# Optimization experiments

Hardware: AMD Instinct MI355X
Metric: run time of the kernel (lower is better)

## Reference

```python
import jax, jax.numpy as jnp
import numpy as np

V, C, S, H, B, T = 10000, 1024, 128, 256, 16, 128
NEG = -1e10


def _mlp(x, w1, b1, w2, b2, wo, bo):
    # ResidualLayer (dropout=0, eval): relu(lin1) -> relu(lin2 + residual), then final Linear
    h = jax.nn.relu(x @ w1 + b1)
    h = jax.nn.relu(h @ w2 + b2 + x)
    return h @ wo + bo


def setup_inputs() -> dict:
    key = jax.random.key(0)
    ks = iter(jax.random.split(key, 32))
    d = {}
    d["text"] = jax.random.randint(next(ks), (B, T), 0, V)
    d["word2state"] = jax.random.randint(next(ks), (V, S), 0, C)

    def rn(shape, scale):
        return jax.random.normal(next(ks), shape, dtype=jnp.float32) * scale

    s = 1.0 / np.sqrt(H)
    d["start_emb"] = rn((C, H), 1.0)
    d["start_w1"], d["start_b1"] = rn((H, H), s), jnp.zeros((H,), jnp.float32)
    d["start_w2"], d["start_b2"] = rn((H, H), s), jnp.zeros((H,), jnp.float32)
    d["start_wo"], d["start_bo"] = rn((H, 1), s), jnp.zeros((1,), jnp.float32)
    d["state_emb"] = rn((C, H), 1.0)
    d["trans_w1"], d["trans_b1"] = rn((H, H), s), jnp.zeros((H,), jnp.float32)
    d["trans_w2"], d["trans_b2"] = rn((H, H), s), jnp.zeros((H,), jnp.float32)
    d["trans_wo"], d["trans_bo"] = rn((H, C), s), jnp.zeros((C,), jnp.float32)
    d["pre_emb"] = rn((C, H), 1.0)
    d["term_w1"], d["term_b1"] = rn((H, H), s), jnp.zeros((H,), jnp.float32)
    d["term_w2"], d["term_b2"] = rn((H, H), s), jnp.zeros((H,), jnp.float32)
    d["term_wo"], d["term_bo"] = rn((H, V), s), jnp.zeros((V,), jnp.float32)
    return d


def _evidence(text, word2state,
              start_emb, start_w1, start_b1, start_w2, start_b2, start_wo, start_bo,
              state_emb, trans_w1, trans_b1, trans_w2, trans_b2, trans_wo, trans_bo,
              pre_emb, term_w1, term_b1, term_w2, term_b2, term_wo, term_bo):
    # start distribution over C states
    start = jax.nn.log_softmax(
        _mlp(start_emb, start_w1, start_b1, start_w2, start_b2, start_wo, start_bo)[:, 0])
    # transition [C, C]
    transition = jax.nn.log_softmax(
        _mlp(state_emb, trans_w1, trans_b1, trans_w2, trans_b2, trans_wo, trans_bo), axis=-1)
    # emission with sparse state->word mask (scatter of word2state)
    em_logits = _mlp(pre_emb, term_w1, term_b1, term_w2, term_b2, term_wo, term_bo)  # [C, V]
    a = jnp.repeat(jnp.arange(V), S)  # word index per (word, slot)
    mask = jnp.zeros((C, V), dtype=bool).at[word2state.reshape(-1), a].set(True)
    emission = jax.nn.log_softmax(jnp.where(mask, em_logits, NEG), axis=-1)  # [C, V]

    clamped = word2state[text]  # [B, T, S] states allowed per token
    init = start[clamped[:, 0]]  # [B, S]
    # transition restricted to clamped states: [B, T-1, S_prev, S_next]
    lp = transition[clamped[:, :-1, :, None], clamped[:, 1:, None, :]]
    obs = emission[clamped, text[:, :, None]]  # [B, T, S]
    lp = lp + obs[:, 1:, None, :]                     # emission of next token
    lp = lp.at[:, 0].add(init[:, :, None] + obs[:, 0, :, None])
    lp = jnp.swapaxes(lp, -1, -2)  # [B, T-1, S_next, S_prev]

    # forward algorithm (log-space scan)
    alpha = jax.nn.logsumexp(lp[:, 0], axis=-1)  # [B, S]
    pots = jnp.swapaxes(lp[:, 1:], 0, 1)  # [T-2, B, S, S]

    def step(a_prev, pot):
        return jax.nn.logsumexp(pot + a_prev[:, None, :], axis=-1), None

    alpha_T, _ = jax.lax.scan(step, alpha, pots)
    return jax.nn.logsumexp(alpha_T, axis=-1).sum()


def reference(text, word2state,
              start_emb, start_w1, start_b1, start_w2, start_b2, start_wo, start_bo,
              state_emb, trans_w1, trans_b1, trans_w2, trans_b2, trans_wo, trans_bo,
              pre_emb, term_w1, term_b1, term_w2, term_b2, term_wo, term_bo):
    return _evidence(text, word2state,
                     start_emb, start_w1, start_b1, start_w2, start_b2, start_wo, start_bo,
                     state_emb, trans_w1, trans_b1, trans_w2, trans_b2, trans_wo, trans_bo,
                     pre_emb, term_w1, term_b1, term_w2, term_b2, term_wo, term_bo)
```

## Files before the change

kernel.cpp:

```cpp
#include <hip/hip_runtime.h>
#include <hip/hip_bf16.h>

#define V 10000
#define VP 10112
#define C 1024
#define S 128
#define H 256
#define B 16
#define T 128
#define NR 64
#define CHUNK 158
#define NRP 158
#define LDK 40
#define PITCH 136

typedef unsigned short u16;
typedef unsigned int u32;
typedef __bf16 bf16x8 __attribute__((ext_vector_type(8)));
typedef float f32x4 __attribute__((ext_vector_type(4)));

static __device__ __forceinline__ float bf2f(u16 x){ return __uint_as_float(((u32)x)<<16); }
static __device__ __forceinline__ u16 f2bf(float f){ u32 u=__float_as_uint(f); return (u16)((u + 0x7FFFu + ((u>>16)&1u))>>16); }

struct Cvt3 { const float* s0; const float* s1; const float* s2; u16* d0; u16* d1; u16* d2; };
__global__ __launch_bounds__(256) void k_cvt3(Cvt3 a){
  const float* s = (blockIdx.y==0)? a.s0 : (blockIdx.y==1)? a.s1 : a.s2;
  u16* d = (blockIdx.y==0)? a.d0 : (blockIdx.y==1)? a.d1 : a.d2;
  int i = (blockIdx.x*256 + threadIdx.x)*8;
  float4 x0 = *(const float4*)(s+i);
  float4 x1 = *(const float4*)(s+i+4);
  u16 h[8] = {f2bf(x0.x),f2bf(x0.y),f2bf(x0.z),f2bf(x0.w),f2bf(x1.x),f2bf(x1.y),f2bf(x1.z),f2bf(x1.w)};
  *(uint4*)(d+i) = *(uint4*)h;
}

__global__ __launch_bounds__(256) void k_transpose(const float* __restrict__ src, u16* __restrict__ dst, int N){
  __shared__ float tile[32][33];
  int v0 = blockIdx.x*32, k0 = blockIdx.y*32;
  int tx = threadIdx.x, ty = threadIdx.y;
  for (int i=0;i<32;i+=8){
    int k = k0+ty+i, v = v0+tx;
    tile[ty+i][tx] = (v < N) ? src[(size_t)k*N + v] : 0.f;
  }
  __syncthreads();
  for (int i=0;i<32;i+=8){
    int v = v0+ty+i, k = k0+tx;
    dst[(size_t)v*H + k] = f2bf(tile[tx][ty+i]);
  }
}

struct T6 { const float* s[6]; u16* d[6]; };
__global__ __launch_bounds__(256) void k_transpose6(T6 a){
  const float* src = a.s[blockIdx.z];
  u16* dst = a.d[blockIdx.z];
  __shared__ float tile[32][33];
  int v0 = blockIdx.x*32, k0 = blockIdx.y*32;
  int tx = threadIdx.x, ty = threadIdx.y;
  for (int i=0;i<32;i+=8){
    int k = k0+ty+i, v = v0+tx;
    tile[ty+i][tx] = src[(size_t)k*H + v];
  }
  __syncthreads();
  for (int i=0;i<32;i+=8){
    int v = v0+ty+i, k = k0+tx;
    dst[(size_t)v*H + k] = f2bf(tile[tx][ty+i]);
  }
}

struct M3 { const u16* A[3]; const u16* W[3]; const float* bias[3]; const u16* R[3]; u16* O[3]; };
template<int RESID>
__global__ __launch_bounds__(256) void k_mlpg(M3 a){
  const int z = blockIdx.z;
  const u16* A  = a.A[z];
  const u16* BT = a.W[z];
  const float* bias = a.bias[z];
  const u16* Rm = a.R[z];
  u16* O = a.O[z];
  __shared__ u16 As[128*LDK];
  __shared__ u16 Bs[128*LDK];
  const int tid = threadIdx.x;
  const int lane = tid & 63, wave = tid >> 6;
  const int wm = wave >> 1, wn = wave & 1;
  const int m0 = blockIdx.y * 128, n0 = blockIdx.x * 128;
  const int lr = lane & 15, lg = lane >> 4;
  f32x4 acc[4][4] = {};
  const int sr = tid >> 1, sh = (tid & 1) * 16;
  for (int ks = 0; ks < H; ks += 32){
    const u16* ga = A  + (size_t)(m0 + sr)*H + ks + sh;
    const u16* gb = BT + (size_t)(n0 + sr)*H + ks + sh;
    uint4 a0 = *(const uint4*)ga;
    uint4 a1 = *(const uint4*)(ga + 8);
    uint4 b0 = *(const uint4*)gb;
    uint4 b1 = *(const uint4*)(gb + 8);
    __syncthreads();
    *(uint4*)&As[sr*LDK + sh]     = a0;
    *(uint4*)&As[sr*LDK + sh + 8] = a1;
    *(uint4*)&Bs[sr*LDK + sh]     = b0;
    *(uint4*)&Bs[sr*LDK + sh + 8] = b1;
    __syncthreads();
    bf16x8 af[4], bfr[4];
    #pragma unroll
    for (int m=0;m<4;m++) af[m]  = *(const bf16x8*)&As[(wm*64 + m*16 + lr)*LDK + lg*8];
    #pragma unroll
    for (int n=0;n<4;n++) bfr[n] = *(const bf16x8*)&Bs[(wn*64 + n*16 + lr)*LDK + lg*8];
    #pragma unroll
    for (int m=0;m<4;m++)
      #pragma unroll
      for (int n=0;n<4;n++)
        acc[m][n] = __builtin_amdgcn_mfma_f32_16x16x32_bf16(af[m], bfr[n], acc[m][n], 0,0,0);
  }
  #pragma unroll
  for (int m=0;m<4;m++){
    int r_g = m0 + wm*64 + m*16 + lg*4;
    #pragma unroll
    for (int n=0;n<4;n++){
      int n_g = n0 + wn*64 + n*16 + lr;
      float bv = bias[n_g];
      #pragma unroll
      for (int reg=0; reg<4; reg++){
        int r = r_g + reg;
        float val = acc[m][n][reg] + bv;
        if (RESID) val += bf2f(Rm[(size_t)r*H + n_g]);
        val = fmaxf(val, 0.f);
        O[(size_t)r*H + n_g] = f2bf(val);
      }
    }
  }
}

__global__ __launch_bounds__(1024) void k_start(
    const u16* __restrict__ h2, const float* __restrict__ wo, const float* __restrict__ bo,
    float* __restrict__ start_lp){
  const int c = threadIdx.x;
  const int lane = c & 63, wid = c >> 6;
  __shared__ float red[16];
  __shared__ float Ms, Zs;
  float acc = bo[0];
  const u16* row = h2 + (size_t)c*H;
  for (int k=0;k<H;k+=8){
    uint4 hv = *(const uint4*)(row+k);
    float4 w0 = *(const float4*)(wo+k);
    float4 w1 = *(const float4*)(wo+k+4);
    acc = fmaf(bf2f((u16)(hv.x&0xFFFFu)), w0.x, acc);
    acc = fmaf(bf2f((u16)(hv.x>>16)),     w0.y, acc);
    acc = fmaf(bf2f((u16)(hv.y&0xFFFFu)), w0.z, acc);
    acc = fmaf(bf2f((u16)(hv.y>>16)),     w0.w, acc);
    acc = fmaf(bf2f((u16)(hv.z&0xFFFFu)), w1.x, acc);
    acc = fmaf(bf2f((u16)(hv.z>>16)),     w1.y, acc);
    acc = fmaf(bf2f((u16)(hv.w&0xFFFFu)), w1.z, acc);
    acc = fmaf(bf2f((u16)(hv.w>>16)),     w1.w, acc);
  }
  float m = acc;
  for (int o=1;o<64;o<<=1) m = fmaxf(m, __shfl_xor(m,o));
  if (lane==0) red[wid]=m;
  __syncthreads();
  if (c==0){ float t=red[0]; for(int i=1;i<16;i++) t=fmaxf(t,red[i]); Ms=t; }
  __syncthreads();
  float M = Ms;
  float e = expf(acc - M);
  float sum = e;
  for (int o=1;o<64;o<<=1) sum += __shfl_xor(sum,o);
  __syncthreads();
  if (lane==0) red[wid]=sum;
  __syncthreads();
  if (c==0){ float t=0.f; for(int i=0;i<16;i++) t+=red[i]; Zs=t; }
  __syncthreads();
  start_lp[c] = acc - (M + logf(Zs));
}

template<int BIAS_ROW, int BF16OUT, int COLMAX>
__global__ __launch_bounds__(256) void k_gemm(
    const u16* __restrict__ A, const u16* __restrict__ BT,
    const float* __restrict__ bias, int biasBound,
    void* __restrict__ outp, int ldout, float* __restrict__ cmax){
  __shared__ u16 As[128*LDK];
  __shared__ u16 Bs[128*LDK];
  const int tid = threadIdx.x;
  const int lane = tid & 63, wave = tid >> 6;
  const int wm = wave >> 1, wn = wave & 1;
  const int m0 = blockIdx.y * 128, n0 = blockIdx.x * 128;
  const int lr = lane & 15, lg = lane >> 4;
  f32x4 acc[4][4] = {};
  const int sr = tid >> 1, sh = (tid & 1) * 16;
  for (int ks = 0; ks < H; ks += 32){
    const u16* ga = A  + (size_t)(m0 + sr)*H + ks + sh;
    const u16* gb = BT + (size_t)(n0 + sr)*H + ks + sh;
    uint4 a0 = *(const uint4*)ga;
    uint4 a1 = *(const uint4*)(ga + 8);
    uint4 b0 = *(const uint4*)gb;
    uint4 b1 = *(const uint4*)(gb + 8);
    __syncthreads();
    *(uint4*)&As[sr*LDK + sh]     = a0;
    *(uint4*)&As[sr*LDK + sh + 8] = a1;
    *(uint4*)&Bs[sr*LDK + sh]     = b0;
    *(uint4*)&Bs[sr*LDK + sh + 8] = b1;
    __syncthreads();
    bf16x8 af[4], bfr[4];
    #pragma unroll
    for (int m=0;m<4;m++) af[m]  = *(const bf16x8*)&As[(wm*64 + m*16 + lr)*LDK + lg*8];
    #pragma unroll
    for (int n=0;n<4;n++) bfr[n] = *(const bf16x8*)&Bs[(wn*64 + n*16 + lr)*LDK + lg*8];
    #pragma unroll
    for (int m=0;m<4;m++)
      #pragma unroll
      for (int n=0;n<4;n++)
        acc[m][n] = __builtin_amdgcn_mfma_f32_16x16x32_bf16(af[m], bfr[n], acc[m][n], 0,0,0);
  }
  float cmx[4] = {-1e30f,-1e30f,-1e30f,-1e30f};
  #pragma unroll
  for (int m=0;m<4;m++){
    int r_g = m0 + wm*64 + m*16 + lg*4;
    #pragma unroll
    for (int n=0;n<4;n++){
      int n_g = n0 + wn*64 + n*16 + lr;
      float bcol = BIAS_ROW ? 0.f : bias[n_g];
      #pragma unroll
      for (int reg=0; reg<4; reg++){
        int r = r_g + reg;
        float bv = BIAS_ROW ? ((r < biasBound) ? bias[r] : 0.f) : bcol;
        float val = acc[m][n][reg] + bv;
        if (COLMAX) cmx[n] = fmaxf(cmx[n], val);
        if (BF16OUT) ((u16*)outp)[(size_t)r*ldout + n_g] = f2bf(val);
        else         ((float*)outp)[(size_t)r*ldout + n_g] = val;
      }
    }
  }
  if (COLMAX){
    #pragma unroll
    for (int n=0;n<4;n++){
      float m_ = cmx[n];
      m_ = fmaxf(m_, __shfl_xor(m_,16));
      m_ = fmaxf(m_, __shfl_xor(m_,32));
      if (lg==0) cmax[((size_t)(blockIdx.y*2 + wm))*C + n0 + wn*64 + n*16 + lr] = m_;
    }
  }
}

__global__ __launch_bounds__(256) void k_softmax(const float* __restrict__ TL, u16* __restrict__ P){
  const int c = blockIdx.x;
  const int tid = threadIdx.x, lane = tid & 63, wid = tid >> 6;
  __shared__ float red[4];
  __shared__ float Ms, Zs;
  float4 v = ((const float4*)(TL + (size_t)c*C))[tid];
  float m = fmaxf(fmaxf(v.x,v.y), fmaxf(v.z,v.w));
  for (int o=1;o<64;o<<=1) m = fmaxf(m, __shfl_xor(m,o));
  if (lane==0) red[wid] = m;
  __syncthreads();
  if (tid==0) Ms = fmaxf(fmaxf(red[0],red[1]), fmaxf(red[2],red[3]));
  __syncthreads();
  float M = Ms;
  float e0 = expf(v.x-M), e1 = expf(v.y-M), e2 = expf(v.z-M), e3 = expf(v.w-M);
  float s = (e0+e1)+(e2+e3);
  for (int o=1;o<64;o<<=1) s += __shfl_xor(s,o);
  if (lane==0) red[wid] = s;
  __syncthreads();
  if (tid==0) Zs = red[0]+red[1]+red[2]+red[3];
  __syncthreads();
  float inv = 1.f/Zs;
  u32 lo = (u32)f2bf(e0*inv) | ((u32)f2bf(e1*inv)<<16);
  u32 hi = (u32)f2bf(e2*inv) | ((u32)f2bf(e3*inv)<<16);
  *(uint2*)(P + (size_t)c*C + tid*4) = make_uint2(lo, hi);
}

__global__ void k_shiftc(const float* __restrict__ shiftp, float* __restrict__ shift){
  int c = threadIdx.x + blockIdx.x*blockDim.x;
  if (c < C){
    float m = -1e30f;
    for (int r=0;r<NRP;r++) m = fmaxf(m, shiftp[(size_t)r*C + c]);
    shift[c] = m;
  }
}

__global__ __launch_bounds__(256) void k_scatter(
    const int* __restrict__ w2s, const u16* __restrict__ EM,
    const float* __restrict__ shift, u16* __restrict__ D){
  int idx = blockIdx.x*256 + threadIdx.x;
  int v = idx >> 7;
  const int c = w2s[idx];
  float val = bf2f(EM[(size_t)v*C + c]);
  D[(size_t)v*C + c] = f2bf(expf(val - shift[c]));
}

__global__ __launch_bounds__(256) void k_colsum(const u16* __restrict__ D, float* __restrict__ sumexp){
  const int c = blockIdx.x*256 + threadIdx.x;
  const int v0 = blockIdx.y*CHUNK;
  float s = 0.f;
  const u16* p = D + (size_t)v0*C + c;
  #pragma unroll 2
  for (int i=0;i<CHUNK;i++){ s += bf2f(p[0]); p += C; }
  sumexp[(size_t)blockIdx.y*C + c] = s;
}

__global__ void k_lse(const float* __restrict__ shift, const float* __restrict__ sumexp, float* __restrict__ lse){
  int c = threadIdx.x + blockIdx.x*blockDim.x;
  if (c < C){
    float s = 0.f;
    for (int r=0;r<NR;r++) s += sumexp[(size_t)r*C + c];
    lse[c] = shift[c] + logf(s);
  }
}

__global__ __launch_bounds__(128) void k_obs(
    const int* __restrict__ text, const int* __restrict__ w2s,
    const u16* __restrict__ EM, const float* __restrict__ lse,
    float* __restrict__ obs){
  const int bt = blockIdx.x;
  const int s = threadIdx.x;
  const int v = text[bt];
  const int c = w2s[(size_t)v*S + s];
  obs[(size_t)bt*S + s] = bf2f(EM[(size_t)v*C + c]) - lse[c];
}

__global__ __launch_bounds__(256) void k_pair0(
    const int* __restrict__ text, const int* __restrict__ w2s,
    const float* __restrict__ start_lp, const float* __restrict__ obs,
    const u16* __restrict__ P, u16* __restrict__ out, float* __restrict__ scales){
  const int j = blockIdx.x;
  const int b = blockIdx.y;
  const int t0 = 2*j, t1 = 2*j+1;
  __shared__ __align__(16) u16 tile[128*PITCH];
  __shared__ int cp0[S], cn0[S], cp1[S], cn1[S];
  __shared__ float eo0[S], eo1[S], a00[S];
  __shared__ float red[4];
  const int tid = threadIdx.x;
  if (tid < 128){
    int s = tid;
    int cpv = w2s[(size_t)text[b*T + t0]*S + s];
    cp0[s] = cpv;
    cn0[s] = w2s[(size_t)text[b*T + t0+1]*S + s];
    eo0[s] = expf(obs[((size_t)b*T + t0 + 1)*S + s]);
    a00[s] = (t0==0) ? expf(start_lp[cpv] + obs[(size_t)(b*T)*S + s]) : 1.0f;
  } else if (t1 < 127){
    int s = tid-128;
    cp1[s] = w2s[(size_t)text[b*T + t1]*S + s];
    cn1[s] = w2s[(size_t)text[b*T + t1+1]*S + s];
    eo1[s] = expf(obs[((size_t)b*T + t1 + 1)*S + s]);
  }
  __syncthreads();
  const int sn = tid & 127, half = tid >> 7;
  const int lane = tid & 63, wave = tid >> 6;
  const int wm = wave >> 1, wn = wave & 1;
  const int lr = lane & 15, lg = lane >> 4;
  {
    const float e = eo0[sn];
    const int cnv = cn0[sn];
    for (int it=0; it<64; ++it){
      int sp = it*2 + half;
      float v = bf2f(P[(size_t)cp0[sp]*C + cnv]) * e * a00[sp];
      tile[sp*PITCH + sn] = f2bf(v);
    }
  }
  __syncthreads();
  bf16x8 bfr[4][4];
  #pragma unroll
  for (int n=0;n<4;n++)
    #pragma unroll
    for (int kc=0;kc<4;kc++)
      bfr[n][kc] = *(const bf16x8*)&tile[(wn*64+n*16+lr)*PITCH + kc*32 + lg*8];
  __syncthreads();
  if (t1 < 127){
    const float e = eo1[sn];
    const int cnv = cn1[sn];
    #pragma unroll
    for (int g=0; g<8; ++g){
      u16 h[8];
      #pragma unroll
      for (int q=0; q<8; ++q){
        int sp = half*64 + g*8 + q;
        h[q] = f2bf(bf2f(P[(size_t)cp1[sp]*C + cnv]) * e);
      }
      *(uint4*)&tile[sn*PITCH + half*64 + g*8] = *(uint4*)h;
    }
  } else {
    #pragma unroll
    for (int g=0; g<8; ++g){
      u16 h[8];
      #pragma unroll
      for (int q=0; q<8; ++q){
        int sp = half*64 + g*8 + q;
        h[q] = (sn == sp) ? (u16)0x3F80u : (u16)0u;
      }
      *(uint4*)&tile[sn*PITCH + half*64 + g*8] = *(uint4*)h;
    }
  }
  __syncthreads();
  f32x4 acc[4][4] = {};
  #pragma unroll
  for (int kc=0; kc<4; ++kc){
    bf16x8 af[4];
    #pragma unroll
    for (int m=0;m<4;m++) af[m] = *(const bf16x8*)&tile[(wm*64+m*16+lr)*PITCH + kc*32 + lg*8];
    #pragma unroll
    for (int m=0;m<4;m++)
      #pragma unroll
      for (int n=0;n<4;n++)
        acc[m][n] = __builtin_amdgcn_mfma_f32_16x16x32_bf16(af[m], bfr[n][kc], acc[m][n], 0,0,0);
  }
  float mx = 0.f;
  #pragma unroll
  for (int m=0;m<4;m++)
    #pragma unroll
    for (int n=0;n<4;n++)
      #pragma unroll
      for (int r=0;r<4;r++) mx = fmaxf(mx, acc[m][n][r]);
  for (int o=1;o<64;o<<=1) mx = fmaxf(mx, __shfl_xor(mx,o));
  if (lane==0) red[wave] = mx;
  __syncthreads();
  mx = fmaxf(fmaxf(red[0],red[1]), fmaxf(red[2],red[3]));
  const float sc = 1.0f / mx;
  if (tid==0) scales[(size_t)b*127 + j] = logf(mx);
  u16* Cg = out + ((size_t)b*64 + j)*(S*S);
  if (j & 1){
    #pragma unroll
    for (int m=0;m<4;m++){
      int rg = wm*64 + m*16 + lg*4;
      #pragma unroll
      for (int n=0;n<4;n++){
        int cg = wn*64 + n*16 + lr;
        #pragma unroll
        for (int r=0;r<4;r++) Cg[(size_t)(rg+r)*128 + cg] = f2bf(acc[m][n][r]*sc);
      }
    }
  } else {
    #pragma unroll
    for (int m=0;m<4;m++){
      int rg = wm*64 + m*16 + lg*4;
      #pragma unroll
      for (int n=0;n<4;n++){
        int cg = wn*64 + n*16 + lr;
        float v0=acc[m][n][0]*sc, v1=acc[m][n][1]*sc, v2=acc[m][n][2]*sc, v3=acc[m][n][3]*sc;
        u32 p0, p1;
        asm("v_cvt_pk_bf16_f32 %0, %1, %2" : "=v"(p0) : "v"(v0), "v"(v1));
        asm("v_cvt_pk_bf16_f32 %0, %1, %2" : "=v"(p1) : "v"(v2), "v"(v3));
        *(uint2*)(Cg + (size_t)cg*128 + rg) = make_uint2(p0, p1);
      }
    }
  }
}

__global__ __launch_bounds__(256) void k_pair(
    const u16* __restrict__ in, u16* __restrict__ out,
    float* __restrict__ scales, int nin, int soff){
  const int j = blockIdx.x;
  const int b = blockIdx.y;
  const int nout = nin >> 1;
  const u16* Ag = in + ((size_t)b*nin + 2*j+1)*(S*S);
  const u16* Bg = in + ((size_t)b*nin + 2*j  )*(S*S);
  u16* Cg = out + ((size_t)b*nout + j)*(S*S);
  const int tid = threadIdx.x;
  const int lane = tid & 63, wave = tid >> 6;
  const int wm = wave >> 1, wn = wave & 1;
  const int lr = lane & 15, lg = lane >> 4;
  f32x4 acc[4][4] = {};
  #pragma unroll
  for (int kc=0; kc<4; ++kc){
    bf16x8 af[4], bfr[4];
    #pragma unroll
    for (int m=0;m<4;m++) af[m]  = *(const bf16x8*)(Ag + (size_t)(wm*64+m*16+lr)*128 + kc*32 + lg*8);
    #pragma unroll
    for (int n=0;n<4;n++) bfr[n] = *(const bf16x8*)(Bg + (size_t)(wn*64+n*16+lr)*128 + kc*32 + lg*8);
    #pragma unroll
    for (int m=0;m<4;m++)
      #pragma unroll
      for (int n=0;n<4;n++)
        acc[m][n] = __builtin_amdgcn_mfma_f32_16x16x32_bf16(af[m], bfr[n], acc[m][n], 0,0,0);
  }
  __shared__ float red[4];
  float mx = 0.f;
  #pragma unroll
  for (int m=0;m<4;m++)
    #pragma unroll
    for (int n=0;n<4;n++)
      #pragma unroll
      for (int r=0;r<4;r++) mx = fmaxf(mx, acc[m][n][r]);
  for (int o=1;o<64;o<<=1) mx = fmaxf(mx, __shfl_xor(mx,o));
  if (lane==0) red[wave] = mx;
  __syncthreads();
  mx = fmaxf(fmaxf(red[0],red[1]), fmaxf(red[2],red[3]));
  const float sc = 1.0f / mx;
  if (tid==0) scales[(size_t)b*127 + soff + j] = logf(mx);
  if (j & 1){
    #pragma unroll
    for (int m=0;m<4;m++){
      int rg = wm*64 + m*16 + lg*4;
      #pragma unroll
      for (int n=0;n<4;n++){
        int cg = wn*64 + n*16 + lr;
        #pragma unroll
        for (int r=0;r<4;r++) Cg[(size_t)(rg+r)*128 + cg] = f2bf(acc[m][n][r]*sc);
      }
    }
  } else {
    #pragma unroll
    for (int m=0;m<4;m++){
      int rg = wm*64 + m*16 + lg*4;
      #pragma unroll
      for (int n=0;n<4;n++){
        int cg = wn*64 + n*16 + lr;
        float v0=acc[m][n][0]*sc, v1=acc[m][n][1]*sc, v2=acc[m][n][2]*sc, v3=acc[m][n][3]*sc;
        u32 p0, p1;
        asm("v_cvt_pk_bf16_f32 %0, %1, %2" : "=v"(p0) : "v"(v0), "v"(v1));
        asm("v_cvt_pk_bf16_f32 %0, %1, %2" : "=v"(p1) : "v"(v2), "v"(v3));
        *(uint2*)(Cg + (size_t)cg*128 + rg) = make_uint2(p0, p1);
      }
    }
  }
}

__global__ __launch_bounds__(256) void k_fin(
    const u16* __restrict__ fin, const float* __restrict__ scales, float* __restrict__ res){
  const int b = blockIdx.x;
  const int tid = threadIdx.x, lane = tid & 63, wid = tid >> 6;
  __shared__ float red[8];
  const u16* p = fin + (size_t)b*(S*S);
  float s = 0.f;
  #pragma unroll
  for (int i=0;i<8;i++){
    uint4 w = *(const uint4*)(p + (i*256+tid)*8);
    s += bf2f((u16)(w.x&0xFFFFu)) + bf2f((u16)(w.x>>16))
       + bf2f((u16)(w.y&0xFFFFu)) + bf2f((u16)(w.y>>16))
       + bf2f((u16)(w.z&0xFFFFu)) + bf2f((u16)(w.z>>16))
       + bf2f((u16)(w.w&0xFFFFu)) + bf2f((u16)(w.w>>16));
  }
  for (int o=1;o<64;o<<=1) s += __shfl_xor(s,o);
  if (lane==0) red[wid] = s;
  float sl = (tid < 127) ? scales[(size_t)b*127 + tid] : 0.f;
  for (int o=1;o<64;o<<=1) sl += __shfl_xor(sl,o);
  if (lane==0) red[4+wid] = sl;
  __syncthreads();
  if (tid==0){
    float tot = red[0]+red[1]+red[2]+red[3];
    float ssum = red[4]+red[5]+red[6]+red[7];
    res[b] = logf(tot) + ssum;
  }
}

__global__ void k_final(const float* __restrict__ res, float* __restrict__ out){
  if (threadIdx.x==0){
    float s = 0.f;
    for (int i=0;i<B;i++) s += res[i];
    out[0] = s;
  }
}

extern "C" void kernel_launch(void* const* d_in, const int* in_sizes, int n_in,
                              void* d_out, int out_size, void* d_ws, size_t ws_size,
                              hipStream_t stream){
  const int*   text      = (const int*)d_in[0];
  const int*   w2s       = (const int*)d_in[1];
  const float* start_emb = (const float*)d_in[2];
  const float* start_w1  = (const float*)d_in[3];
  const float* start_b1  = (const float*)d_in[4];
  const float* start_w2  = (const float*)d_in[5];
  const float* start_b2  = (const float*)d_in[6];
  const float* start_wo  = (const float*)d_in[7];
  const float* start_bo  = (const float*)d_in[8];
  const float* state_emb = (const float*)d_in[9];
  const float* trans_w1  = (const float*)d_in[10];
  const float* trans_b1  = (const float*)d_in[11];
  const float* trans_w2  = (const float*)d_in[12];
  const float* trans_b2  = (const float*)d_in[13];
  const float* trans_wo  = (const float*)d_in[14];
  const float* trans_bo  = (const float*)d_in[15];
  const float* pre_emb   = (const float*)d_in[16];
  const float* term_w1   = (const float*)d_in[17];
  const float* term_b1   = (const float*)d_in[18];
  const float* term_w2   = (const float*)d_in[19];
  const float* term_b2   = (const float*)d_in[20];
  const float* term_wo   = (const float*)d_in[21];
  const float* term_bo   = (const float*)d_in[22];

  char* ws = (char*)d_ws;
  size_t off = 0;
  auto alloc = [&](size_t bytes)->char*{ char* p = ws + off; off += (bytes + 255) & ~(size_t)255; return p; };
  u16*   embb     = (u16*)  alloc(sizeof(u16)*3*(size_t)C*H);
  u16*   h1b      = (u16*)  alloc(sizeof(u16)*3*(size_t)C*H);
  u16*   h2b      = (u16*)  alloc(sizeof(u16)*3*(size_t)C*H);
  u16*   wt       = (u16*)  alloc(sizeof(u16)*6*(size_t)H*H);
  float* start_lp = (float*)alloc(sizeof(float)*C);
  float* shift    = (float*)alloc(sizeof(float)*C);
  float* shiftp   = (float*)alloc(sizeof(float)*(size_t)C*NRP);
  float* sumexp   = (float*)alloc(sizeof(float)*(size_t)C*NR);
  float* lse      = (float*)alloc(sizeof(float)*C);
  float* resb     = (float*)alloc(sizeof(float)*B);
  float* scales   = (float*)alloc(sizeof(float)*(size_t)B*127);
  u16*   P        = (u16*)  alloc(sizeof(u16)*(size_t)C*C);
  u16*   wotb     = (u16*)  alloc(sizeof(u16)*(size_t)VP*H);
  u16*   wottr    = (u16*)  alloc(sizeof(u16)*(size_t)C*H);
  float* obs      = (float*)alloc(sizeof(float)*(size_t)B*T*S);
  u16*   EM       = (u16*)  alloc(sizeof(u16)*(size_t)VP*C);
  u16*   treeA    = (u16*)  alloc(sizeof(u16)*(size_t)B*64*S*S);
  u16*   treeB    = (u16*)  alloc(sizeof(u16)*(size_t)B*32*S*S);
  float* TL       = (float*)treeA;
  u16*   D        = (u16*)((char*)treeA + sizeof(float)*(size_t)C*C);
  (void)ws_size; (void)in_sizes; (void)n_in; (void)out_size;

  u16* embb0 = embb, *embb1 = embb + (size_t)C*H, *embb2 = embb + 2*(size_t)C*H;
  u16* h1b0 = h1b, *h1b1 = h1b + (size_t)C*H, *h1b2 = h1b + 2*(size_t)C*H;
  u16* h2b0 = h2b, *h2b1 = h2b + (size_t)C*H, *h2b2 = h2b + 2*(size_t)C*H;

  hipMemsetAsync(D, 0, sizeof(u16)*(size_t)VP*C, stream);

  Cvt3 cv; cv.s0 = start_emb; cv.s1 = state_emb; cv.s2 = pre_emb;
  cv.d0 = embb0; cv.d1 = embb1; cv.d2 = embb2;
  k_cvt3<<<dim3(C*H/(256*8), 3), dim3(256), 0, stream>>>(cv);

  T6 t6;
  t6.s[0]=start_w1; t6.s[1]=start_w2; t6.s[2]=trans_w1; t6.s[3]=trans_w2; t6.s[4]=term_w1; t6.s[5]=term_w2;
  for (int i=0;i<6;i++) t6.d[i] = wt + (size_t)i*H*H;
  k_transpose6<<<dim3(H/32, H/32, 6), dim3(32,8), 0, stream>>>(t6);

  M3 l1;
  l1.A[0]=embb0; l1.A[1]=embb1; l1.A[2]=embb2;
  l1.W[0]=wt;    l1.W[1]=wt+2*(size_t)H*H; l1.W[2]=wt+4*(size_t)H*H;
  l1.bias[0]=start_b1; l1.bias[1]=trans_b1; l1.bias[2]=term_b1;
  l1.R[0]=l1.R[1]=l1.R[2]=nullptr;
  l1.O[0]=h1b0; l1.O[1]=h1b1; l1.O[2]=h1b2;
  k_mlpg<0><<<dim3(H/128, C/128, 3), dim3(256), 0, stream>>>(l1);

  M3 l2;
  l2.A[0]=h1b0; l2.A[1]=h1b1; l2.A[2]=h1b2;
  l2.W[0]=wt+(size_t)H*H; l2.W[1]=wt+3*(size_t)H*H; l2.W[2]=wt+5*(size_t)H*H;
  l2.bias[0]=start_b2; l2.bias[1]=trans_b2; l2.bias[2]=term_b2;
  l2.R[0]=embb0; l2.R[1]=embb1; l2.R[2]=embb2;
  l2.O[0]=h2b0; l2.O[1]=h2b1; l2.O[2]=h2b2;
  k_mlpg<1><<<dim3(H/128, C/128, 3), dim3(256), 0, stream>>>(l2);

  k_start<<<dim3(1), dim3(1024), 0, stream>>>(h2b0, start_wo, start_bo, start_lp);
  k_transpose<<<dim3(VP/32, H/32), dim3(32,8), 0, stream>>>(term_wo, wotb, V);
  k_transpose<<<dim3(C/32, H/32), dim3(32,8), 0, stream>>>(trans_wo, wottr, C);
  k_gemm<0,0,0><<<dim3(C/128, C/128), dim3(256), 0, stream>>>(h2b1, wottr, trans_bo, C, TL, C, nullptr);
  k_softmax<<<dim3(C), dim3(256), 0, stream>>>(TL, P);
  k_gemm<1,1,1><<<dim3(C/128, VP/128), dim3(256), 0, stream>>>(wotb, h2b2, term_bo, V, EM, C, shiftp);
  k_shiftc<<<dim3((C+255)/256), dim3(256), 0, stream>>>(shiftp, shift);
  k_scatter<<<dim3(V*S/256), dim3(256), 0, stream>>>(w2s, EM, shift, D);
  k_colsum<<<dim3(C/256, NR), dim3(256), 0, stream>>>(D, sumexp);
  k_lse<<<dim3((C+255)/256), dim3(256), 0, stream>>>(shift, sumexp, lse);
  k_obs<<<dim3(B*T), dim3(128), 0, stream>>>(text, w2s, EM, lse, obs);

  k_pair0<<<dim3(64, B), dim3(256), 0, stream>>>(text, w2s, start_lp, obs, P, treeA, scales);

  {
    u16* lin = treeA;
    u16* bufs[2] = { treeB, treeA };
    int nin = 64, soff = 64, cur = 0;
    while (nin > 1){
      int nout = nin >> 1;
      k_pair<<<dim3(nout, B), dim3(256), 0, stream>>>(lin, bufs[cur], scales, nin, soff);
      lin = bufs[cur];
      cur ^= 1;
      soff += nout;
      nin = nout;
    }
    k_fin<<<dim3(B), dim3(256), 0, stream>>>(lin, scales, resb);
  }
  k_final<<<dim3(1), dim3(64), 0, stream>>>(resb, (float*)d_out);
}
```

Baseline: 280.1 us.

## Fuse tree reduction levels into quad kernels and stage gathered rows in LDS

The binary-tree matrix product over time steps now fuses two tree levels per kernel (k_quad), keeping intermediate products in swizzled LDS instead of writing them to global memory. The final three levels are fused into k_fin4, which cuts the launch count from seven kernels to three. k_pair0 now gathers whole P rows with coalesced 16-byte loads into an LDS staging buffer and then picks columns from it, replacing scattered per-element global reads. This adds LDS pressure (64KB per block) and less parallelism at the later levels.

```diff
diff --git a/kernel.cpp b/kernel.cpp
--- a/kernel.cpp
+++ b/kernel.cpp
@@ -12,7 +12,9 @@
 #define CHUNK 158
 #define NRP 158
 #define LDK 40
-#define PITCH 136
+#define SPITCH 1032
+
+#define TIX(r,g) (((r)<<7) + ((((g) ^ ((r)&7)))<<3))
 
 typedef unsigned short u16;
 typedef unsigned int u32;
@@ -317,8 +319,9 @@
   const int j = blockIdx.x;
   const int b = blockIdx.y;
   const int t0 = 2*j, t1 = 2*j+1;
-  __shared__ __align__(16) u16 tile[128*PITCH];
-  __shared__ int cp0[S], cn0[S], cp1[S], cn1[S];
+  __shared__ __align__(16) u16 tile[128*128];
+  __shared__ __align__(16) u16 stage[8*SPITCH];
+  __shared__ int cp0[S], cp1[S], cn1[S];
   __shared__ float eo0[S], eo1[S], a00[S];
   __shared__ float red[4];
   const int tid = threadIdx.x;
@@ -326,69 +329,88 @@
     int s = tid;
     int cpv = w2s[(size_t)text[b*T + t0]*S + s];
     cp0[s] = cpv;
-    cn0[s] = w2s[(size_t)text[b*T + t0+1]*S + s];
+    cp1[s] = w2s[(size_t)text[b*T + t0+1]*S + s];
     eo0[s] = expf(obs[((size_t)b*T + t0 + 1)*S + s]);
     a00[s] = (t0==0) ? expf(start_lp[cpv] + obs[(size_t)(b*T)*S + s]) : 1.0f;
   } else if (t1 < 127){
     int s = tid-128;
-    cp1[s] = w2s[(size_t)text[b*T + t1]*S + s];
     cn1[s] = w2s[(size_t)text[b*T + t1+1]*S + s];
     eo1[s] = expf(obs[((size_t)b*T + t1 + 1)*S + s]);
   }
   __syncthreads();
-  const int sn = tid & 127, half = tid >> 7;
   const int lane = tid & 63, wave = tid >> 6;
   const int wm = wave >> 1, wn = wave & 1;
   const int lr = lane & 15, lg = lane >> 4;
-  {
-    const float e = eo0[sn];
-    const int cnv = cn0[sn];
-    for (int it=0; it<64; ++it){
-      int sp = it*2 + half;
-      float v = bf2f(P[(size_t)cp0[sp]*C + cnv]) * e * a00[sp];
-      tile[sp*PITCH + sn] = f2bf(v);
-    }
-  }
-  __syncthreads();
+  for (int c8 = 0; c8 < 16; ++c8){
+    #pragma unroll
+    for (int p=0;p<4;p++){
+      int idx = p*256 + tid;
+      int r = idx >> 7, col16 = idx & 127;
+      *(uint4*)&stage[r*SPITCH + col16*8] = *(const uint4*)&P[(size_t)cp0[c8*8 + r]*C + col16*8];
+    }
+    __syncthreads();
+    {
+      int r = tid >> 5, kh = tid & 31;
+      float asp = a00[c8*8 + r];
+      u16 h4[4];
+      #pragma unroll
+      for (int q=0;q<4;q++){
+        int k = kh*4 + q;
+        h4[q] = f2bf(bf2f(stage[r*SPITCH + cp1[k]]) * eo0[k] * asp);
+      }
+      *(uint2*)&tile[TIX(c8*8 + r, kh>>1) + (kh&1)*4] = *(uint2*)h4;
+    }
+    __syncthreads();
+  }
   bf16x8 bfr[4][4];
   #pragma unroll
   for (int n=0;n<4;n++)
     #pragma unroll
     for (int kc=0;kc<4;kc++)
-      bfr[n][kc] = *(const bf16x8*)&tile[(wn*64+n*16+lr)*PITCH + kc*32 + lg*8];
+      bfr[n][kc] = *(const bf16x8*)&tile[TIX(wn*64+n*16+lr, kc*4+lg)];
   __syncthreads();
   if (t1 < 127){
+    const int sn = tid & 127, half = tid >> 7;
+    const int cnv = cn1[sn];
     const float e = eo1[sn];
-    const int cnv = cn1[sn];
-    #pragma unroll
-    for (int g=0; g<8; ++g){
-      u16 h[8];
-      #pragma unroll
-      for (int q=0; q<8; ++q){
-        int sp = half*64 + g*8 + q;
-        h[q] = f2bf(bf2f(P[(size_t)cp1[sp]*C + cnv]) * e);
-      }
-      *(uint4*)&tile[sn*PITCH + half*64 + g*8] = *(uint4*)h;
+    for (int c8 = 0; c8 < 16; ++c8){
+      #pragma unroll
+      for (int p=0;p<4;p++){
+        int idx = p*256 + tid;
+        int r = idx >> 7, col16 = idx & 127;
+        *(uint4*)&stage[r*SPITCH + col16*8] = *(const uint4*)&P[(size_t)cp1[c8*8 + r]*C + col16*8];
+      }
+      __syncthreads();
+      {
+        u16 h4[4];
+        #pragma unroll
+        for (int q=0;q<4;q++){
+          int rr = half*4 + q;
+          h4[q] = f2bf(bf2f(stage[rr*SPITCH + cnv]) * e);
+        }
+        *(uint2*)&tile[TIX(sn, c8) + half*4] = *(uint2*)h4;
+      }
+      __syncthreads();
     }
   } else {
-    #pragma unroll
-    for (int g=0; g<8; ++g){
-      u16 h[8];
-      #pragma unroll
-      for (int q=0; q<8; ++q){
-        int sp = half*64 + g*8 + q;
-        h[q] = (sn == sp) ? (u16)0x3F80u : (u16)0u;
-      }
-      *(uint4*)&tile[sn*PITCH + half*64 + g*8] = *(uint4*)h;
-    }
-  }
-  __syncthreads();
+    if (tid < 128){
+      int sn = tid;
+      #pragma unroll
+      for (int g=0; g<16; ++g){
+        u16 h8[8];
+        #pragma unroll
+        for (int q=0;q<8;q++) h8[q] = (g*8+q == sn) ? (u16)0x3F80u : (u16)0u;
+        *(uint4*)&tile[TIX(sn, g)] = *(uint4*)h8;
+      }
+    }
+    __syncthreads();
+  }
   f32x4 acc[4][4] = {};
   #pragma unroll
   for (int kc=0; kc<4; ++kc){
     bf16x8 af[4];
     #pragma unroll
-    for (int m=0;m<4;m++) af[m] = *(const bf16x8*)&tile[(wm*64+m*16+lr)*PITCH + kc*32 + lg*8];
+    for (int m=0;m<4;m++) af[m] = *(const bf16x8*)&tile[TIX(wm*64+m*16+lr, kc*4+lg)];
     #pragma unroll
     for (int m=0;m<4;m++)
       #pragma unroll
@@ -437,34 +459,134 @@
   }
 }
 
-__global__ __launch_bounds__(256) void k_pair(
+__global__ __launch_bounds__(256) void k_quad(
     const u16* __restrict__ in, u16* __restrict__ out,
-    float* __restrict__ scales, int nin, int soff){
-  const int j = blockIdx.x;
+    float* __restrict__ scales, int nin, int soff_i, int soff_o){
+  const int q = blockIdx.x;
   const int b = blockIdx.y;
-  const int nout = nin >> 1;
-  const u16* Ag = in + ((size_t)b*nin + 2*j+1)*(S*S);
-  const u16* Bg = in + ((size_t)b*nin + 2*j  )*(S*S);
-  u16* Cg = out + ((size_t)b*nout + j)*(S*S);
+  const int nout = nin >> 2;
+  const u16* T0 = in + ((size_t)b*nin + 4*q+0)*(S*S);
+  const u16* T1 = in + ((size_t)b*nin + 4*q+1)*(S*S);
+  const u16* T2 = in + ((size_t)b*nin + 4*q+2)*(S*S);
+  const u16* T3 = in + ((size_t)b*nin + 4*q+3)*(S*S);
+  __shared__ __align__(16) u16 ldsA[128*128];
+  __shared__ __align__(16) u16 ldsB[128*128];
+  __shared__ float red[4];
   const int tid = threadIdx.x;
   const int lane = tid & 63, wave = tid >> 6;
   const int wm = wave >> 1, wn = wave & 1;
   const int lr = lane & 15, lg = lane >> 4;
-  f32x4 acc[4][4] = {};
+  f32x4 acc[4][4];
+  #pragma unroll
+  for (int m=0;m<4;m++)
+    #pragma unroll
+    for (int n=0;n<4;n++) acc[m][n] = (f32x4){0.f,0.f,0.f,0.f};
   #pragma unroll
   for (int kc=0; kc<4; ++kc){
-    bf16x8 af[4], bfr[4];
-    #pragma unroll
-    for (int m=0;m<4;m++) af[m]  = *(const bf16x8*)(Ag + (size_t)(wm*64+m*16+lr)*128 + kc*32 + lg*8);
-    #pragma unroll
-    for (int n=0;n<4;n++) bfr[n] = *(const bf16x8*)(Bg + (size_t)(wn*64+n*16+lr)*128 + kc*32 + lg*8);
-    #pragma unroll
-    for (int m=0;m<4;m++)
-      #pragma unroll
-      for (int n=0;n<4;n++)
-        acc[m][n] = __builtin_amdgcn_mfma_f32_16x16x32_bf16(af[m], bfr[n], acc[m][n], 0,0,0);
-  }
-  __shared__ float red[4];
+    bf16x8 af[4], bf[4];
+    #pragma unroll
+    for (int m=0;m<4;m++) af[m] = *(const bf16x8*)(T1 + (size_t)(wm*64+m*16+lr)*128 + kc*32 + lg*8);
+    #pragma unroll
+    for (int n=0;n<4;n++) bf[n] = *(const bf16x8*)(T0 + (size_t)(wn*64+n*16+lr)*128 + kc*32 + lg*8);
+    #pragma unroll
+    for (int m=0;m<4;m++)
+      #pragma unroll
+      for (int n=0;n<4;n++)
+        acc[m][n] = __builtin_amdgcn_mfma_f32_16x16x32_bf16(af[m], bf[n], acc[m][n], 0,0,0);
+  }
+  {
+    float mx = 0.f;
+    #pragma unroll
+    for (int m=0;m<4;m++)
+      #pragma unroll
+      for (int n=0;n<4;n++)
+        #pragma unroll
+        for (int r=0;r<4;r++) mx = fmaxf(mx, acc[m][n][r]);
+    for (int o=1;o<64;o<<=1) mx = fmaxf(mx, __shfl_xor(mx,o));
+    if (lane==0) red[wave] = mx;
+    __syncthreads();
+    mx = fmaxf(fmaxf(red[0],red[1]), fmaxf(red[2],red[3]));
+    float sc = 1.0f/mx;
+    if (tid==0) scales[(size_t)b*127 + soff_i + 2*q] = logf(mx);
+    #pragma unroll
+    for (int m=0;m<4;m++){
+      int rg = wm*64 + m*16 + lg*4;
+      #pragma unroll
+      for (int n=0;n<4;n++){
+        int cg = wn*64 + n*16 + lr;
+        float v0=acc[m][n][0]*sc, v1=acc[m][n][1]*sc, v2=acc[m][n][2]*sc, v3=acc[m][n][3]*sc;
+        u32 p0, p1;
+        asm("v_cvt_pk_bf16_f32 %0, %1, %2" : "=v"(p0) : "v"(v0), "v"(v1));
+        asm("v_cvt_pk_bf16_f32 %0, %1, %2" : "=v"(p1) : "v"(v2), "v"(v3));
+        *(uint2*)&ldsB[TIX(cg, rg>>3) + (rg&7)] = make_uint2(p0, p1);
+      }
+    }
+  }
+  __syncthreads();
+  #pragma unroll
+  for (int m=0;m<4;m++)
+    #pragma unroll
+    for (int n=0;n<4;n++) acc[m][n] = (f32x4){0.f,0.f,0.f,0.f};
+  #pragma unroll
+  for (int kc=0; kc<4; ++kc){
+    bf16x8 af[4], bf[4];
+    #pragma unroll
+    for (int m=0;m<4;m++) af[m] = *(const bf16x8*)(T2 + (size_t)(wm*64+m*16+lr)*128 + kc*32 + lg*8);
+    #pragma unroll
+    for (int n=0;n<4;n++) bf[n] = *(const bf16x8*)(T3 + (size_t)(wn*64+n*16+lr)*128 + kc*32 + lg*8);
+    #pragma unroll
+    for (int m=0;m<4;m++)
+      #pragma unroll
+      for (int n=0;n<4;n++)
+        acc[m][n] = __builtin_amdgcn_mfma_f32_16x16x32_bf16(af[m], bf[n], acc[m][n], 0,0,0);
+  }
+  {
+    float mx = 0.f;
+    #pragma unroll
+    for (int m=0;m<4;m++)
+      #pragma unroll
+      for (int n=0;n<4;n++)
+        #pragma unroll
+        for (int r=0;r<4;r++) mx = fmaxf(mx, acc[m][n][r]);
+    for (int o=1;o<64;o<<=1) mx = fmaxf(mx, __shfl_xor(mx,o));
+    __syncthreads();
+    if (lane==0) red[wave] = mx;
+    __syncthreads();
+    mx = fmaxf(fmaxf(red[0],red[1]), fmaxf(red[2],red[3]));
+    float sc = 1.0f/mx;
+    if (tid==0) scales[(size_t)b*127 + soff_i + 2*q + 1] = logf(mx);
+    #pragma unroll
+    for (int m=0;m<4;m++){
+      int rg = wm*64 + m*16 + lg*4;
+      #pragma unroll
+      for (int n=0;n<4;n++){
+        int cg = wn*64 + n*16 + lr;
+        float v0=acc[m][n][0]*sc, v1=acc[m][n][1]*sc, v2=acc[m][n][2]*sc, v3=acc[m][n][3]*sc;
+        u32 p0, p1;
+        asm("v_cvt_pk_bf16_f32 %0, %1, %2" : "=v"(p0) : "v"(v0), "v"(v1));
+        asm("v_cvt_pk_bf16_f32 %0, %1, %2" : "=v"(p1) : "v"(v2), "v"(v3));
+        *(uint2*)&ldsA[TIX(cg, rg>>3) + (rg&7)] = make_uint2(p0, p1);
+      }
+    }
+  }
+  __syncthreads();
+  #pragma unroll
+  for (int m=0;m<4;m++)
+    #pragma unroll
+    for (int n=0;n<4;n++) acc[m][n] = (f32x4){0.f,0.f,0.f,0.f};
+  #pragma unroll
+  for (int kc=0; kc<4; ++kc){
+    bf16x8 af[4], bf[4];
+    #pragma unroll
+    for (int m=0;m<4;m++) af[m] = *(const bf16x8*)&ldsA[TIX(wm*64+m*16+lr, kc*4+lg)];
+    #pragma unroll
+    for (int n=0;n<4;n++) bf[n] = *(const bf16x8*)&ldsB[TIX(wn*64+n*16+lr, kc*4+lg)];
+    #pragma unroll
+    for (int m=0;m<4;m++)
+      #pragma unroll
+      for (int n=0;n<4;n++)
+        acc[m][n] = __builtin_amdgcn_mfma_f32_16x16x32_bf16(af[m], bf[n], acc[m][n], 0,0,0);
+  }
   float mx = 0.f;
   #pragma unroll
   for (int m=0;m<4;m++)
@@ -473,12 +595,14 @@
       #pragma unroll
       for (int r=0;r<4;r++) mx = fmaxf(mx, acc[m][n][r]);
   for (int o=1;o<64;o<<=1) mx = fmaxf(mx, __shfl_xor(mx,o));
+  __syncthreads();
   if (lane==0) red[wave] = mx;
   __syncthreads();
   mx = fmaxf(fmaxf(red[0],red[1]), fmaxf(red[2],red[3]));
   const float sc = 1.0f / mx;
-  if (tid==0) scales[(size_t)b*127 + soff + j] = logf(mx);
-  if (j & 1){
+  if (tid==0) scales[(size_t)b*127 + soff_o + q] = logf(mx);
+  u16* Cg = out + ((size_t)b*nout + q)*(S*S);
+  if (q & 1){
     #pragma unroll
     for (int m=0;m<4;m++){
       int rg = wm*64 + m*16 + lg*4;
@@ -506,31 +630,149 @@
   }
 }
 
-__global__ __launch_bounds__(256) void k_fin(
-    const u16* __restrict__ fin, const float* __restrict__ scales, float* __restrict__ res){
+__global__ __launch_bounds__(256) void k_fin4(
+    const u16* __restrict__ in, const float* __restrict__ scales, float* __restrict__ res){
   const int b = blockIdx.x;
-  const int tid = threadIdx.x, lane = tid & 63, wid = tid >> 6;
+  const u16* T0 = in + ((size_t)b*4 + 0)*(S*S);
+  const u16* T1 = in + ((size_t)b*4 + 1)*(S*S);
+  const u16* T2 = in + ((size_t)b*4 + 2)*(S*S);
+  const u16* T3 = in + ((size_t)b*4 + 3)*(S*S);
+  __shared__ __align__(16) u16 ldsA[128*128];
+  __shared__ __align__(16) u16 ldsB[128*128];
   __shared__ float red[8];
-  const u16* p = fin + (size_t)b*(S*S);
+  __shared__ float sloc[2];
+  const int tid = threadIdx.x;
+  const int lane = tid & 63, wave = tid >> 6;
+  const int wm = wave >> 1, wn = wave & 1;
+  const int lr = lane & 15, lg = lane >> 4;
+  f32x4 acc[4][4];
+  #pragma unroll
+  for (int m=0;m<4;m++)
+    #pragma unroll
+    for (int n=0;n<4;n++) acc[m][n] = (f32x4){0.f,0.f,0.f,0.f};
+  #pragma unroll
+  for (int kc=0; kc<4; ++kc){
+    bf16x8 af[4], bf[4];
+    #pragma unroll
+    for (int m=0;m<4;m++) af[m] = *(const bf16x8*)(T1 + (size_t)(wm*64+m*16+lr)*128 + kc*32 + lg*8);
+    #pragma unroll
+    for (int n=0;n<4;n++) bf[n] = *(const bf16x8*)(T0 + (size_t)(wn*64+n*16+lr)*128 + kc*32 + lg*8);
+    #pragma unroll
+    for (int m=0;m<4;m++)
+      #pragma unroll
+      for (int n=0;n<4;n++)
+        acc[m][n] = __builtin_amdgcn_mfma_f32_16x16x32_bf16(af[m], bf[n], acc[m][n], 0,0,0);
+  }
+  {
+    float mx = 0.f;
+    #pragma unroll
+    for (int m=0;m<4;m++)
+      #pragma unroll
+      for (int n=0;n<4;n++)
+        #pragma unroll
+        for (int r=0;r<4;r++) mx = fmaxf(mx, acc[m][n][r]);
+    for (int o=1;o<64;o<<=1) mx = fmaxf(mx, __shfl_xor(mx,o));
+    if (lane==0) red[wave] = mx;
+    __syncthreads();
+    mx = fmaxf(fmaxf(red[0],red[1]), fmaxf(red[2],red[3]));
+    float sc = 1.0f/mx;
+    if (tid==0) sloc[0] = logf(mx);
+    #pragma unroll
+    for (int m=0;m<4;m++){
+      int rg = wm*64 + m*16 + lg*4;
+      #pragma unroll
+      for (int n=0;n<4;n++){
+        int cg = wn*64 + n*16 + lr;
+        float v0=acc[m][n][0]*sc, v1=acc[m][n][1]*sc, v2=acc[m][n][2]*sc, v3=acc[m][n][3]*sc;
+        u32 p0, p1;
+        asm("v_cvt_pk_bf16_f32 %0, %1, %2" : "=v"(p0) : "v"(v0), "v"(v1));
+        asm("v_cvt_pk_bf16_f32 %0, %1, %2" : "=v"(p1) : "v"(v2), "v"(v3));
+        *(uint2*)&ldsB[TIX(cg, rg>>3) + (rg&7)] = make_uint2(p0, p1);
+      }
+    }
+  }
+  __syncthreads();
+  #pragma unroll
+  for (int m=0;m<4;m++)
+    #pragma unroll
+    for (int n=0;n<4;n++) acc[m][n] = (f32x4){0.f,0.f,0.f,0.f};
+  #pragma unroll
+  for (int kc=0; kc<4; ++kc){
+    bf16x8 af[4], bf[4];
+    #pragma unroll
+    for (int m=0;m<4;m++) af[m] = *(const bf16x8*)(T2 + (size_t)(wm*64+m*16+lr)*128 + kc*32 + lg*8);
+    #pragma unroll
+    for (int n=0;n<4;n++) bf[n] = *(const bf16x8*)(T3 + (size_t)(wn*64+n*16+lr)*128 + kc*32 + lg*8);
+    #pragma unroll
+    for (int m=0;m<4;m++)
+      #pragma unroll
+      for (int n=0;n<4;n++)
+        acc[m][n] = __builtin_amdgcn_mfma_f32_16x16x32_bf16(af[m], bf[n], acc[m][n], 0,0,0);
+  }
+  {
+    float mx = 0.f;
+    #pragma unroll
+    for (int m=0;m<4;m++)
+      #pragma unroll
+      for (int n=0;n<4;n++)
+        #pragma unroll
+        for (int r=0;r<4;r++) mx = fmaxf(mx, acc[m][n][r]);
+    for (int o=1;o<64;o<<=1) mx = fmaxf(mx, __shfl_xor(mx,o));
+    __syncthreads();
+    if (lane==0) red[wave] = mx;
+    __syncthreads();
+    mx = fmaxf(fmaxf(red[0],red[1]), fmaxf(red[2],red[3]));
+    float sc = 1.0f/mx;
+    if (tid==0) sloc[1] = logf(mx);
+    #pragma unroll
+    for (int m=0;m<4;m++){
+      int rg = wm*64 + m*16 + lg*4;
+      #pragma unroll
+      for (int n=0;n<4;n++){
+        int cg = wn*64 + n*16 + lr;
+        float v0=acc[m][n][0]*sc, v1=acc[m][n][1]*sc, v2=acc[m][n][2]*sc, v3=acc[m][n][3]*sc;
+        u32 p0, p1;
+        asm("v_cvt_pk_bf16_f32 %0, %1, %2" : "=v"(p0) : "v"(v0), "v"(v1));
+        asm("v_cvt_pk_bf16_f32 %0, %1, %2" : "=v"(p1) : "v"(v2), "v"(v3));
+        *(uint2*)&ldsA[TIX(cg, rg>>3) + (rg&7)] = make_uint2(p0, p1);
+      }
+    }
+  }
+  __syncthreads();
+  #pragma unroll
+  for (int m=0;m<4;m++)
+    #pragma unroll
+    for (int n=0;n<4;n++) acc[m][n] = (f32x4){0.f,0.f,0.f,0.f};
+  #pragma unroll
+  for (int kc=0; kc<4; ++kc){
+    bf16x8 af[4], bf[4];
+    #pragma unroll
+    for (int m=0;m<4;m++) af[m] = *(const bf16x8*)&ldsA[TIX(wm*64+m*16+lr, kc*4+lg)];
+    #pragma unroll
+    for (int n=0;n<4;n++) bf[n] = *(const bf16x8*)&ldsB[TIX(wn*64+n*16+lr, kc*4+lg)];
+    #pragma unroll
+    for (int m=0;m<4;m++)
+      #pragma unroll
+      for (int n=0;n<4;n++)
+        acc[m][n] = __builtin_amdgcn_mfma_f32_16x16x32_bf16(af[m], bf[n], acc[m][n], 0,0,0);
+  }
   float s = 0.f;
   #pragma unroll
-  for (int i=0;i<8;i++){
-    uint4 w = *(const uint4*)(p + (i*256+tid)*8);
-    s += bf2f((u16)(w.x&0xFFFFu)) + bf2f((u16)(w.x>>16))
-       + bf2f((u16)(w.y&0xFFFFu)) + bf2f((u16)(w.y>>16))
-       + bf2f((u16)(w.z&0xFFFFu)) + bf2f((u16)(w.z>>16))
-       + bf2f((u16)(w.w&0xFFFFu)) + bf2f((u16)(w.w>>16));
-  }
+  for (int m=0;m<4;m++)
+    #pragma unroll
+    for (int n=0;n<4;n++)
+      #pragma unroll
+      for (int r=0;r<4;r++) s += acc[m][n][r];
   for (int o=1;o<64;o<<=1) s += __shfl_xor(s,o);
-  if (lane==0) red[wid] = s;
-  float sl = (tid < 127) ? scales[(size_t)b*127 + tid] : 0.f;
+  float sl = (tid < 124) ? scales[(size_t)b*127 + tid] : 0.f;
   for (int o=1;o<64;o<<=1) sl += __shfl_xor(sl,o);
-  if (lane==0) red[4+wid] = sl;
+  __syncthreads();
+  if (lane==0){ red[wave] = s; red[4+wave] = sl; }
   __syncthreads();
   if (tid==0){
-    float tot = red[0]+red[1]+red[2]+red[3];
+    float tot  = red[0]+red[1]+red[2]+red[3];
     float ssum = red[4]+red[5]+red[6]+red[7];
-    res[b] = logf(tot) + ssum;
+    res[b] = logf(tot) + ssum + sloc[0] + sloc[1];
   }
 }
 
@@ -589,7 +831,7 @@
   float* obs      = (float*)alloc(sizeof(float)*(size_t)B*T*S);
   u16*   EM       = (u16*)  alloc(sizeof(u16)*(size_t)VP*C);
   u16*   treeA    = (u16*)  alloc(sizeof(u16)*(size_t)B*64*S*S);
-  u16*   treeB    = (u16*)  alloc(sizeof(u16)*(size_t)B*32*S*S);
+  u16*   treeB    = (u16*)  alloc(sizeof(u16)*(size_t)B*16*S*S);
   float* TL       = (float*)treeA;
   u16*   D        = (u16*)((char*)treeA + sizeof(float)*(size_t)C*C);
   (void)ws_size; (void)in_sizes; (void)n_in; (void)out_size;
@@ -638,20 +880,8 @@
   k_obs<<<dim3(B*T), dim3(128), 0, stream>>>(text, w2s, EM, lse, obs);
 
   k_pair0<<<dim3(64, B), dim3(256), 0, stream>>>(text, w2s, start_lp, obs, P, treeA, scales);
-
-  {
-    u16* lin = treeA;
-    u16* bufs[2] = { treeB, treeA };
-    int nin = 64, soff = 64, cur = 0;
-    while (nin > 1){
-      int nout = nin >> 1;
-      k_pair<<<dim3(nout, B), dim3(256), 0, stream>>>(lin, bufs[cur], scales, nin, soff);
-      lin = bufs[cur];
-      cur ^= 1;
-      soff += nout;
-      nin = nout;
-    }
-    k_fin<<<dim3(B), dim3(256), 0, stream>>>(lin, scales, resb);
-  }
+  k_quad<<<dim3(16, B), dim3(256), 0, stream>>>(treeA, treeB, scales, 64, 64, 96);
+  k_quad<<<dim3(4,  B), dim3(256), 0, stream>>>(treeB, treeA, scales, 16, 112, 120);
+  k_fin4<<<dim3(B), dim3(256), 0, stream>>>(treeA, scales, resb);
   k_final<<<dim3(1), dim3(64), 0, stream>>>(resb, (float*)d_out);
 }
```

Result: no change. 277.4 us (-0.9%).
